# Kernel tuning notes

Measured on AMD Instinct MI355X. Metric: run time of the kernel, lower is better.

## Reference

```python
import jax, jax.numpy as jnp
import numpy as np

N = 100000   # total nodes
E = 1600000  # total edges
B = 256      # graphs per batch
F_NODE, F_EDGE, H = 35, 10, 64
N_CONV = 3
IN_DIM = 2 * H + F_EDGE  # 138
EPS = 1e-5


def setup_inputs() -> dict:
    key = jax.random.key(0)
    ks = jax.random.split(key, 16)
    node_features = jax.random.normal(ks[0], (N, F_NODE), dtype=jnp.float32)
    edge_index = jax.random.randint(ks[1], (2, E), 0, N, dtype=jnp.int64)
    edge_features = jax.random.uniform(ks[2], (E, F_EDGE), dtype=jnp.float32)
    graph_index = jnp.sort(jax.random.randint(ks[3], (N,), 0, B, dtype=jnp.int64))
    s = lambda fan_in: 1.0 / np.sqrt(fan_in)
    embed_w = jax.random.uniform(ks[4], (F_NODE, H), jnp.float32, -s(F_NODE), s(F_NODE))
    embed_b = jax.random.uniform(ks[5], (H,), jnp.float32, -s(F_NODE), s(F_NODE))
    gate_w = jax.random.uniform(ks[6], (N_CONV, IN_DIM, H), jnp.float32, -s(IN_DIM), s(IN_DIM))
    gate_b = jax.random.uniform(ks[7], (N_CONV, H), jnp.float32, -s(IN_DIM), s(IN_DIM))
    cand_w = jax.random.uniform(ks[8], (N_CONV, IN_DIM, H), jnp.float32, -s(IN_DIM), s(IN_DIM))
    cand_b = jax.random.uniform(ks[9], (N_CONV, H), jnp.float32, -s(IN_DIM), s(IN_DIM))
    bn_g = jnp.ones((N_CONV, H), dtype=jnp.float32)
    bn_b = jnp.zeros((N_CONV, H), dtype=jnp.float32)
    mlp_w1 = jax.random.uniform(ks[10], (H, 128), jnp.float32, -s(H), s(H))
    mlp_b1 = jax.random.uniform(ks[11], (128,), jnp.float32, -s(H), s(H))
    mlp_w2 = jax.random.uniform(ks[12], (128, 64), jnp.float32, -s(128), s(128))
    mlp_b2 = jax.random.uniform(ks[13], (64,), jnp.float32, -s(128), s(128))
    mlp_w3 = jax.random.uniform(ks[14], (64, 1), jnp.float32, -s(64), s(64))
    mlp_b3 = jax.random.uniform(ks[15], (1,), jnp.float32, -s(64), s(64))
    return dict(node_features=node_features, edge_index=edge_index,
                edge_features=edge_features, graph_index=graph_index,
                embed_w=embed_w, embed_b=embed_b,
                gate_w=gate_w, gate_b=gate_b, cand_w=cand_w, cand_b=cand_b,
                bn_g=bn_g, bn_b=bn_b,
                mlp_w1=mlp_w1, mlp_b1=mlp_b1, mlp_w2=mlp_w2, mlp_b2=mlp_b2,
                mlp_w3=mlp_w3, mlp_b3=mlp_b3)


def _conv(h, src, dst, edge_feat, gw, gb, cw, cb, gamma, beta):
    # gather -> concat -> gated message
    z = jnp.concatenate([h[src], h[dst], edge_feat], axis=1)  # [E, 2H+F_edge]
    g = jax.nn.sigmoid(z @ gw + gb)
    c = jax.nn.softplus(z @ cw + cb)
    m = g * c
    # scatter-add onto source nodes
    agg = jax.ops.segment_sum(m, src, num_segments=h.shape[0])
    # BatchNorm1d (training-mode batch stats, biased variance)
    mu = agg.mean(axis=0)
    var = agg.var(axis=0)
    agg_bn = (agg - mu) * jax.lax.rsqrt(var + EPS) * gamma + beta
    return jax.nn.softplus(h + agg_bn)


def reference(node_features, edge_index, edge_features, graph_index,
              embed_w, embed_b, gate_w, gate_b, cand_w, cand_b, bn_g, bn_b,
              mlp_w1, mlp_b1, mlp_w2, mlp_b2, mlp_w3, mlp_b3):
    src, dst = edge_index[0], edge_index[1]
    h = node_features @ embed_w + embed_b  # [N, H]
    for i in range(N_CONV):
        h = _conv(h, src, dst, edge_features,
                  gate_w[i], gate_b[i], cand_w[i], cand_b[i], bn_g[i], bn_b[i])
    # mean pool per graph (B is static = 256)
    pooled = jax.ops.segment_sum(h, graph_index, num_segments=B)
    counts = jax.ops.segment_sum(jnp.ones((h.shape[0],), h.dtype), graph_index, num_segments=B)
    pooled = pooled / jnp.clip(counts, 1.0, None)[:, None]
    x = jax.nn.softplus(pooled @ mlp_w1 + mlp_b1)
    x = jax.nn.softplus(x @ mlp_w2 + mlp_b2)
    return (x @ mlp_w3 + mlp_b3)[:, 0]  # [B]
```

## Files before the change

### kernel.cpp

```cpp
#include <hip/hip_runtime.h>
#include <hip/hip_bf16.h>

#define NN 100000
#define EE 1600000
#define BB 256
#define F_NODE 35
#define F_EDGE 10
#define HH 64
#define IN_DIM 138
#define N_CONV 3
#define EPSBN 1e-5f
#define NB1 ((NN + 255) / 256)

#define NBLK 6144
#define NGROUPS 17
#define SUBLEN 68
#define EPB 272
#define EPADTOT (NBLK * EPB)
#define NPAD (EPADTOT - EE)
#define EFSTR 12

#define LOG2E 1.442695041f
#define LN2   0.6931471806f

typedef _Float16 half8 __attribute__((ext_vector_type(8)));
typedef float floatx4 __attribute__((ext_vector_type(4)));

__device__ __forceinline__ float softplus_fast(float x) {
    float t = __builtin_amdgcn_exp2f(fminf(LOG2E * x, 126.0f));
    return LN2 * __builtin_amdgcn_logf(1.0f + t);
}
__device__ __forceinline__ float mpair_pre(float g2, float c2) {
    float tg = __builtin_amdgcn_exp2f(g2);
    float sig = __builtin_amdgcn_rcpf(1.0f + tg);
    float tc = __builtin_amdgcn_exp2f(fminf(c2, 126.0f));
    float l = __builtin_amdgcn_logf(1.0f + tc);
    return sig * l;
}

__global__ __launch_bounds__(256)
void hist_rank_kernel(const int* __restrict__ src, int* __restrict__ cnt,
                      int* __restrict__ rank) {
    int e = blockIdx.x * 256 + threadIdx.x;
    rank[e] = atomicAdd(&cnt[src[e]], 1);
}

__global__ __launch_bounds__(256)
void scan1_kernel(int* __restrict__ cnt, int* __restrict__ bsum, int n) {
    __shared__ int ls[256];
    int t = threadIdx.x;
    int i = blockIdx.x * 256 + t;
    int v = (i < n) ? cnt[i] : 0;
    ls[t] = v;
    __syncthreads();
#pragma unroll
    for (int off = 1; off < 256; off <<= 1) {
        int add = (t >= off) ? ls[t - off] : 0;
        __syncthreads();
        ls[t] += add;
        __syncthreads();
    }
    if (i < n) cnt[i] = ls[t] - v;
    if (t == 255) bsum[blockIdx.x] = ls[255];
}

__global__ __launch_bounds__(512)
void scan2_kernel(int* __restrict__ bsum, int nb) {
    __shared__ int ls[512];
    int t = threadIdx.x;
    int v = (t < nb) ? bsum[t] : 0;
    ls[t] = v;
    __syncthreads();
#pragma unroll
    for (int off = 1; off < 512; off <<= 1) {
        int add = (t >= off) ? ls[t - off] : 0;
        __syncthreads();
        ls[t] += add;
        __syncthreads();
    }
    if (t < nb) bsum[t] = ls[t] - v;
}

__global__ __launch_bounds__(256)
void perm_kernel(const int* __restrict__ src, const int* __restrict__ rank,
                 const int* __restrict__ offs, const int* __restrict__ bsum,
                 int* __restrict__ perm) {
    int e = blockIdx.x * 256 + threadIdx.x;
    int s = src[e];
    perm[offs[s] + bsum[s >> 8] + rank[e]] = e;
}

__global__ __launch_bounds__(256)
void gather_kernel(const int* __restrict__ perm,
                   const int* __restrict__ src, const int* __restrict__ dst,
                   const float* __restrict__ ef,
                   int* __restrict__ ssorted, int2* __restrict__ sdsorted,
                   _Float16* __restrict__ ef16) {
    int pos = blockIdx.x * 256 + threadIdx.x;
    int e = perm[pos];
    int s = src[e], d = dst[e];
    ssorted[pos] = s;
    int2 sd; sd.x = s; sd.y = d;
    sdsorted[pos] = sd;
    const float2* efe = (const float2*)(ef + (size_t)e * F_EDGE);
    uint* op = (uint*)(ef16 + (size_t)pos * EFSTR);
#pragma unroll
    for (int i = 0; i < 5; i++) {
        float2 v = efe[i];
        _Float16 h0 = (_Float16)v.x;
        _Float16 h1 = (_Float16)v.y;
        op[i] = (uint)*(unsigned short*)&h0 | ((uint)*(unsigned short*)&h1 << 16);
    }
    op[5] = 0u;
}

__global__ __launch_bounds__(256)
void pad_kernel(int* __restrict__ ssorted, int2* __restrict__ sdsorted,
                _Float16* __restrict__ ef16, _Float16* __restrict__ h16) {
    int t = blockIdx.x * 256 + threadIdx.x;
    int pos = EE + t;
    ssorted[pos] = NN;
    int2 sd; sd.x = NN; sd.y = NN;
    sdsorted[pos] = sd;
    uint2 z2; z2.x = 0u; z2.y = 0u;
    uint2* op = (uint2*)(ef16 + (size_t)pos * EFSTR);
    op[0] = z2; op[1] = z2; op[2] = z2;
    if (t < 32) ((uint2*)(h16 + (size_t)NN * HH))[t] = z2;
}

__global__ __launch_bounds__(256)
void prep_w_kernel(const float* __restrict__ gw, const float* __restrict__ cw,
                   _Float16* __restrict__ wT) {
    int idx = blockIdx.x * 256 + threadIdx.x;
    if (idx >= 3 * 128 * 160) return;
    int k = idx % 160;
    int n = (idx / 160) & 127;
    int layer = idx / (160 * 128);
    float v = 0.f;
    if (k < IN_DIM)
        v = (n < 64) ? (-LOG2E) * gw[layer * IN_DIM * HH + k * HH + n]
                     : ( LOG2E) * cw[layer * IN_DIM * HH + k * HH + (n - 64)];
    wT[idx] = (_Float16)v;
}

__global__ __launch_bounds__(256)
void embed_kernel(const float* __restrict__ nf, const float* __restrict__ w,
                  const float* __restrict__ bias, _Float16* __restrict__ h16, int n) {
    __shared__ float wl[F_NODE * HH];
    int tid = threadIdx.x;
    for (int i = tid; i < F_NODE * HH; i += 256) wl[i] = w[i];
    __syncthreads();
    int idx = blockIdx.x * 256 + tid;
    int node = idx >> 6, j = idx & 63;
    if (node >= n) return;
    float acc = bias[j];
    const float* row = nf + node * F_NODE;
#pragma unroll
    for (int k = 0; k < F_NODE; k++) acc += row[k] * wl[k * HH + j];
    h16[idx] = (_Float16)acc;
}

__device__ __forceinline__ void loadA(uint4* A,
                                      const _Float16* __restrict__ h16,
                                      const _Float16* __restrict__ ef16,
                                      int s, int d, int eg, int quad) {
    const uint4* hs = (const uint4*)(h16 + (size_t)s * HH);
    const uint4* hd = (const uint4*)(h16 + (size_t)d * HH);
    A[0] = hs[quad];
    A[1] = hs[quad + 4];
    A[2] = hd[quad];
    A[3] = hd[quad + 4];
    uint4 z; z.x = z.y = z.z = z.w = 0u;
    A[4] = z;
    const _Float16* p = ef16 + (size_t)eg * EFSTR;
    if (quad == 0) {
        uint2 a = *(const uint2*)p;
        uint2 b = *(const uint2*)(p + 4);
        A[4].x = a.x; A[4].y = a.y; A[4].z = b.x; A[4].w = b.y;
    } else if (quad == 1) {
        uint2 a = *(const uint2*)(p + 8);
        A[4].x = a.x; A[4].y = a.y;
    }
}

__global__ __launch_bounds__(128, 3)
void edge_conv_mfma(const _Float16* __restrict__ h16,
                    const int* __restrict__ ssorted,
                    const int2* __restrict__ sdsorted,
                    const _Float16* __restrict__ ef16,
                    const _Float16* __restrict__ wT,
                    const float* __restrict__ gb, const float* __restrict__ cb,
                    float* __restrict__ agg) {
    int lane = threadIdx.x & 63;
    int w = threadIdx.x >> 6;
    int quad = lane >> 4, n15 = lane & 15;
    int blockE = blockIdx.x * EPB;
    int base = blockE + ((n15 >> 2) * SUBLEN) + (n15 & 3);
    int ebase_epi = blockE + quad * SUBLEN;

    int tg = 2 * w;
    half8 B[4][5];
#pragma unroll
    for (int j = 0; j < 2; j++) {
        const _Float16* wrg = wT + ((tg + j) * 16 + n15) * 160 + quad * 8;
        const _Float16* wrc = wT + ((4 + tg + j) * 16 + n15) * 160 + quad * 8;
#pragma unroll
        for (int ks = 0; ks < 5; ks++) {
            B[j][ks]     = *(const half8*)(wrg + ks * 32);
            B[2 + j][ks] = *(const half8*)(wrc + ks * 32);
        }
    }
    float gb0 = -LOG2E * gb[tg * 16 + n15], gb1 = -LOG2E * gb[(tg + 1) * 16 + n15];
    float cb0 =  LOG2E * cb[tg * 16 + n15], cb1 =  LOG2E * cb[(tg + 1) * 16 + n15];
    int colbase = tg * 16 + n15;

    int sprev = -1;
    float am0 = 0.f, am1 = 0.f;

    uint4 A[5];
    {
        int2 sd0 = sdsorted[base];
        loadA(A, h16, ef16, sd0.x, sd0.y, base, quad);
    }
    int2 sdn = sdsorted[base + 4];

    for (int g = 0; g < NGROUPS; g++) {
        int4 ss = *(const int4*)&ssorted[ebase_epi + g * 4];

        floatx4 acc[4];
        acc[0] = (floatx4){gb0, gb0, gb0, gb0};
        acc[1] = (floatx4){gb1, gb1, gb1, gb1};
        acc[2] = (floatx4){cb0, cb0, cb0, cb0};
        acc[3] = (floatx4){cb1, cb1, cb1, cb1};

#pragma unroll
        for (int ks = 0; ks < 5; ks++) {
            half8 a = __builtin_bit_cast(half8, A[ks]);
#pragma unroll
            for (int t = 0; t < 4; t++)
                acc[t] = __builtin_amdgcn_mfma_f32_16x16x32_f16(a, B[t][ks], acc[t], 0, 0, 0);
        }

        int gl = (g + 1 < NGROUPS) ? g + 1 : NGROUPS - 1;
        loadA(A, h16, ef16, sdn.x, sdn.y, base + gl * 4, quad);
        int gp = (g + 2 < NGROUPS) ? g + 2 : NGROUPS - 1;
        sdn = sdsorted[base + gp * 4];

        float mm0[4], mm1[4];
#pragma unroll
        for (int r = 0; r < 4; r++) {
            mm0[r] = mpair_pre(acc[0][r], acc[2][r]);
            mm1[r] = mpair_pre(acc[1][r], acc[3][r]);
        }
        int srr[4] = {ss.x, ss.y, ss.z, ss.w};
#pragma unroll
        for (int r = 0; r < 4; r++) {
            int sr = srr[r];
            if (sr != sprev) {
                if (sprev >= 0) {
                    float* p = agg + (size_t)sprev * HH + colbase;
                    atomicAdd(p, am0);
                    atomicAdd(p + 16, am1);
                }
                sprev = sr;
                am0 = am1 = 0.f;
            }
            am0 = fmaf(mm0[r], LN2, am0);
            am1 = fmaf(mm1[r], LN2, am1);
        }
    }
    if (sprev >= 0) {
        float* p = agg + (size_t)sprev * HH + colbase;
        atomicAdd(p, am0);
        atomicAdd(p + 16, am1);
    }
}

__global__ __launch_bounds__(256)
void bn_stats_kernel(const float* __restrict__ agg, float* __restrict__ stats, int total) {
    __shared__ float ls[256], lss[256];
    int tid = threadIdx.x;
    float s = 0.f, ss = 0.f;
    for (int idx = blockIdx.x * 256 + tid; idx < total; idx += gridDim.x * 256) {
        float v = agg[idx];
        s += v;
        ss += v * v;
    }
    ls[tid] = s;
    lss[tid] = ss;
    __syncthreads();
    if (tid < 64) {
        s = ls[tid] + ls[tid + 64] + ls[tid + 128] + ls[tid + 192];
        ss = lss[tid] + lss[tid + 64] + lss[tid + 128] + lss[tid + 192];
        atomicAdd(&stats[tid], s);
        atomicAdd(&stats[64 + tid], ss);
    }
}

__global__ __launch_bounds__(256)
void bn_update_kernel(_Float16* __restrict__ h16,
                      float* __restrict__ agg,
                      const float* __restrict__ stats,
                      const float* __restrict__ g, const float* __restrict__ b,
                      int total, float invN) {
    int idx = blockIdx.x * 256 + threadIdx.x;
    if (idx >= total) return;
    int j = idx & 63;
    float mu = stats[j] * invN;
    float var = stats[64 + j] * invN - mu * mu;
    var = fmaxf(var, 0.0f);
    float scale = g[j] * rsqrtf(var + EPSBN);
    float a = agg[idx];
    agg[idx] = 0.f;
    float v = (float)h16[idx] + (a - mu) * scale + b[j];
    h16[idx] = (_Float16)softplus_fast(v);
}

__global__ __launch_bounds__(256)
void pool_kernel(const _Float16* __restrict__ h16, const int* __restrict__ gi,
                 float* __restrict__ pool, float* __restrict__ counts, int n) {
    int tid = threadIdx.x;
    int grp = tid >> 6;
    int j = tid & 63;
    int n0 = blockIdx.x * 64 + grp * 16;
    if (n0 >= n) return;
    int nend = n0 + 16; if (nend > n) nend = n;
    int gprev = gi[n0];
    float a = 0.f;
    int cnt = 0;
    for (int nn = n0; nn < nend; nn++) {
        int gg = gi[nn];
        if (gg != gprev) {
            atomicAdd(&pool[gprev * 64 + j], a);
            if (j == 0) atomicAdd(&counts[gprev], (float)cnt);
            a = 0.f; cnt = 0; gprev = gg;
        }
        a += (float)h16[(size_t)nn * 64 + j];
        cnt++;
    }
    atomicAdd(&pool[gprev * 64 + j], a);
    if (j == 0) atomicAdd(&counts[gprev], (float)cnt);
}

__global__ __launch_bounds__(128)
void mlp_kernel(const float* __restrict__ pool, const float* __restrict__ counts,
                const float* __restrict__ w1, const float* __restrict__ b1,
                const float* __restrict__ w2, const float* __restrict__ b2,
                const float* __restrict__ w3, const float* __restrict__ b3,
                float* __restrict__ out) {
    __shared__ float x0[64], x1[128], x2[64];
    int b = blockIdx.x, t = threadIdx.x;
    if (t < 64) {
        float c = counts[b];
        c = c < 1.f ? 1.f : c;
        x0[t] = pool[b * 64 + t] / c;
    }
    __syncthreads();
    {
        float acc = 0.f;
#pragma unroll
        for (int k = 0; k < 64; k++) acc += x0[k] * w1[k * 128 + t];
        x1[t] = softplus_fast(acc + b1[t]);
    }
    __syncthreads();
    if (t < 64) {
        float acc = 0.f;
#pragma unroll
        for (int k = 0; k < 128; k++) acc += x1[k] * w2[k * 64 + t];
        x2[t] = softplus_fast(acc + b2[t]);
    }
    __syncthreads();
    if (t == 0) {
        float acc = 0.f;
        for (int k = 0; k < 64; k++) acc += x2[k] * w3[k];
        out[b] = acc + b3[0];
    }
}

extern "C" void kernel_launch(void* const* d_in, const int* in_sizes, int n_in,
                              void* d_out, int out_size, void* d_ws, size_t ws_size,
                              hipStream_t stream) {
    const float* nf      = (const float*)d_in[0];
    const int*   ei      = (const int*)d_in[1];
    const float* ef      = (const float*)d_in[2];
    const int*   gi      = (const int*)d_in[3];
    const float* embed_w = (const float*)d_in[4];
    const float* embed_b = (const float*)d_in[5];
    const float* gate_w  = (const float*)d_in[6];
    const float* gate_b  = (const float*)d_in[7];
    const float* cand_w  = (const float*)d_in[8];
    const float* cand_b  = (const float*)d_in[9];
    const float* bn_g    = (const float*)d_in[10];
    const float* bn_b    = (const float*)d_in[11];
    const float* w1      = (const float*)d_in[12];
    const float* b1      = (const float*)d_in[13];
    const float* w2      = (const float*)d_in[14];
    const float* b2      = (const float*)d_in[15];
    const float* w3      = (const float*)d_in[16];
    const float* b3      = (const float*)d_in[17];
    float* out = (float*)d_out;

    const int NH = NN * HH;
    char* p = (char*)d_ws;
    int*       offs    = (int*)p;              p += (size_t)NN * 4;
    float*     agg     = (float*)p;            p += (size_t)(NN + 1) * HH * 4;
    float*     stats   = (float*)p;            p += 3 * 128 * 4;
    float*     pool    = (float*)p;            p += (size_t)BB * HH * 4;
    float*     counts  = (float*)p;            p += (size_t)BB * 4;
    size_t zero_bytes = (size_t)(p - (char*)d_ws);
    _Float16*  h16     = (_Float16*)p;         p += (size_t)(NN + 1) * HH * 2;
    int*       ssorted = (int*)p;              p += (size_t)EPADTOT * 4;
    int2*      sdsorted= (int2*)p;             p += (size_t)EPADTOT * 8;
    _Float16*  ef16    = (_Float16*)p;         p += (size_t)EPADTOT * EFSTR * 2;
    int*       perm    = (int*)p;              p += (size_t)EE * 4;
    int*       rank    = (int*)p;              p += (size_t)EE * 4;
    _Float16*  wTall   = (_Float16*)p;         p += (size_t)3 * 128 * 160 * 2;
    int*       bsum    = (int*)p;              p += 512 * 4;

    const int* src = ei;
    const int* dst = ei + EE;

    hipMemsetAsync(d_ws, 0, zero_bytes, stream);

    hist_rank_kernel<<<EE / 256, 256, 0, stream>>>(src, offs, rank);
    prep_w_kernel<<<(3 * 128 * 160 + 255) / 256, 256, 0, stream>>>(gate_w, cand_w, wTall);
    pad_kernel<<<NPAD / 256, 256, 0, stream>>>(ssorted, sdsorted, ef16, h16);
    scan1_kernel<<<NB1, 256, 0, stream>>>(offs, bsum, NN);
    scan2_kernel<<<1, 512, 0, stream>>>(bsum, NB1);
    perm_kernel<<<EE / 256, 256, 0, stream>>>(src, rank, offs, bsum, perm);
    gather_kernel<<<EE / 256, 256, 0, stream>>>(perm, src, dst, ef, ssorted, sdsorted, ef16);

    embed_kernel<<<NH / 256, 256, 0, stream>>>(nf, embed_w, embed_b, h16, NN);

    for (int i = 0; i < N_CONV; i++) {
        edge_conv_mfma<<<NBLK, 128, 0, stream>>>(
            h16, ssorted, sdsorted, ef16,
            wTall + (size_t)i * 128 * 160,
            gate_b + i * HH, cand_b + i * HH, agg);
        bn_stats_kernel<<<512, 256, 0, stream>>>(agg, stats + i * 128, NH);
        bn_update_kernel<<<NH / 256, 256, 0, stream>>>(
            h16, agg, stats + i * 128, bn_g + i * HH, bn_b + i * HH, NH, 1.0f / (float)NN);
    }

    pool_kernel<<<(NN + 63) / 64, 256, 0, stream>>>(h16, gi, pool, counts, NN);
    mlp_kernel<<<BB, 128, 0, stream>>>(pool, counts, w1, b1, w2, b2, w3, b3, out);
}
```

Measured before the change: 964.8 us.

## Double-buffer edge gathers two groups ahead and enlarge per-block edge tiles

Halves the block count and doubles edges per block (34 groups of 4 per sub-lane), so the per-block weight-fragment loads and the final atomic flush are amortised over more edges. The main loop is unrolled by two with two A buffers, prefetching gathered node/edge rows two groups ahead and indices four ahead to hide gather latency. The occupancy hint in launch bounds is removed and the padding sentinel check becomes an unsigned range test. Extra registers for the second buffer may lower occupancy, and fewer blocks may balance less evenly across CUs.

```diff
diff --git a/kernel.cpp b/kernel.cpp
--- a/kernel.cpp
+++ b/kernel.cpp
@@ -12,10 +12,10 @@
 #define EPSBN 1e-5f
 #define NB1 ((NN + 255) / 256)
 
-#define NBLK 6144
-#define NGROUPS 17
-#define SUBLEN 68
-#define EPB 272
+#define NBLK 3072
+#define NGROUPS 34
+#define SUBLEN 136
+#define EPB 544
 #define EPADTOT (NBLK * EPB)
 #define NPAD (EPADTOT - EE)
 #define EFSTR 12
@@ -183,7 +183,7 @@
     }
 }
 
-__global__ __launch_bounds__(128, 3)
+__global__ __launch_bounds__(128)
 void edge_conv_mfma(const _Float16* __restrict__ h16,
                     const int* __restrict__ ssorted,
                     const int2* __restrict__ sdsorted,
@@ -217,59 +217,69 @@
     int sprev = -1;
     float am0 = 0.f, am1 = 0.f;
 
-    uint4 A[5];
+    uint4 A0[5], A1[5];
+    int2 sdn0, sdn1;
     {
-        int2 sd0 = sdsorted[base];
-        loadA(A, h16, ef16, sd0.x, sd0.y, base, quad);
-    }
-    int2 sdn = sdsorted[base + 4];
-
-    for (int g = 0; g < NGROUPS; g++) {
-        int4 ss = *(const int4*)&ssorted[ebase_epi + g * 4];
-
-        floatx4 acc[4];
-        acc[0] = (floatx4){gb0, gb0, gb0, gb0};
-        acc[1] = (floatx4){gb1, gb1, gb1, gb1};
-        acc[2] = (floatx4){cb0, cb0, cb0, cb0};
-        acc[3] = (floatx4){cb1, cb1, cb1, cb1};
-
-#pragma unroll
-        for (int ks = 0; ks < 5; ks++) {
-            half8 a = __builtin_bit_cast(half8, A[ks]);
-#pragma unroll
-            for (int t = 0; t < 4; t++)
-                acc[t] = __builtin_amdgcn_mfma_f32_16x16x32_f16(a, B[t][ks], acc[t], 0, 0, 0);
+        int2 a = sdsorted[base];
+        int2 b = sdsorted[base + 4];
+        loadA(A0, h16, ef16, a.x, a.y, base, quad);
+        loadA(A1, h16, ef16, b.x, b.y, base + 4, quad);
+        sdn0 = sdsorted[base + 8];
+        sdn1 = sdsorted[base + 12];
+    }
+
+    for (int g = 0; g < NGROUPS; g += 2) {
+#pragma unroll
+        for (int k = 0; k < 2; k++) {
+            int gk = g + k;
+            int4 ss = *(const int4*)&ssorted[ebase_epi + gk * 4];
+
+            floatx4 acc[4];
+            acc[0] = (floatx4){gb0, gb0, gb0, gb0};
+            acc[1] = (floatx4){gb1, gb1, gb1, gb1};
+            acc[2] = (floatx4){cb0, cb0, cb0, cb0};
+            acc[3] = (floatx4){cb1, cb1, cb1, cb1};
+
+#pragma unroll
+            for (int ks = 0; ks < 5; ks++) {
+                half8 a = __builtin_bit_cast(half8, k == 0 ? A0[ks] : A1[ks]);
+#pragma unroll
+                for (int t = 0; t < 4; t++)
+                    acc[t] = __builtin_amdgcn_mfma_f32_16x16x32_f16(a, B[t][ks], acc[t], 0, 0, 0);
+            }
+
+            int gl = (gk + 2 < NGROUPS) ? gk + 2 : NGROUPS - 1;
+            if (k == 0) loadA(A0, h16, ef16, sdn0.x, sdn0.y, base + gl * 4, quad);
+            else        loadA(A1, h16, ef16, sdn1.x, sdn1.y, base + gl * 4, quad);
+            int gp = (gk + 4 < NGROUPS) ? gk + 4 : NGROUPS - 1;
+            int2 sdf = sdsorted[base + gp * 4];
+            if (k == 0) sdn0 = sdf; else sdn1 = sdf;
+
+            float mm0[4], mm1[4];
+#pragma unroll
+            for (int r = 0; r < 4; r++) {
+                mm0[r] = mpair_pre(acc[0][r], acc[2][r]);
+                mm1[r] = mpair_pre(acc[1][r], acc[3][r]);
+            }
+            int srr[4] = {ss.x, ss.y, ss.z, ss.w};
+#pragma unroll
+            for (int r = 0; r < 4; r++) {
+                int sr = srr[r];
+                if (sr != sprev) {
+                    if ((unsigned)sprev < (unsigned)NN) {
+                        float* p = agg + (size_t)sprev * HH + colbase;
+                        atomicAdd(p, am0);
+                        atomicAdd(p + 16, am1);
+                    }
+                    sprev = sr;
+                    am0 = am1 = 0.f;
+                }
+                am0 = fmaf(mm0[r], LN2, am0);
+                am1 = fmaf(mm1[r], LN2, am1);
+            }
         }
-
-        int gl = (g + 1 < NGROUPS) ? g + 1 : NGROUPS - 1;
-        loadA(A, h16, ef16, sdn.x, sdn.y, base + gl * 4, quad);
-        int gp = (g + 2 < NGROUPS) ? g + 2 : NGROUPS - 1;
-        sdn = sdsorted[base + gp * 4];
-
-        float mm0[4], mm1[4];
-#pragma unroll
-        for (int r = 0; r < 4; r++) {
-            mm0[r] = mpair_pre(acc[0][r], acc[2][r]);
-            mm1[r] = mpair_pre(acc[1][r], acc[3][r]);
-        }
-        int srr[4] = {ss.x, ss.y, ss.z, ss.w};
-#pragma unroll
-        for (int r = 0; r < 4; r++) {
-            int sr = srr[r];
-            if (sr != sprev) {
-                if (sprev >= 0) {
-                    float* p = agg + (size_t)sprev * HH + colbase;
-                    atomicAdd(p, am0);
-                    atomicAdd(p + 16, am1);
-                }
-                sprev = sr;
-                am0 = am1 = 0.f;
-            }
-            am0 = fmaf(mm0[r], LN2, am0);
-            am1 = fmaf(mm1[r], LN2, am1);
-        }
-    }
-    if (sprev >= 0) {
+    }
+    if ((unsigned)sprev < (unsigned)NN) {
         float* p = agg + (size_t)sprev * HH + colbase;
         atomicAdd(p, am0);
         atomicAdd(p + 16, am1);
```

After: 852.0 us. 1.13x faster.

## Fuse prep, scan, BN and pool+MLP kernels using grid barriers; double edge block size

Applied to the files above, without the earlier changes.

Merges the embed, histogram, weight-prep and pad kernels into one multi-role launch, and the two scans into one using a last-block-done pattern. BN stats and update are fused with a spin-based grid barrier over 512 blocks, and pooling and the MLP are fused the same way. It also halves the edge-conv block count while doubling edges per block, and filters padding sources with an unsigned bound check. The aim is fewer launches and launch gaps. The cost is spin-barrier risk, since every block must be co-resident, and a different per-block load balance in the edge conv.

```diff
diff --git a/kernel.cpp b/kernel.cpp
--- a/kernel.cpp
+++ b/kernel.cpp
@@ -12,13 +12,21 @@
 #define EPSBN 1e-5f
 #define NB1 ((NN + 255) / 256)
 
-#define NBLK 6144
-#define NGROUPS 17
-#define SUBLEN 68
-#define EPB 272
+#define NBLK 3072
+#define NGROUPS 34
+#define SUBLEN 136
+#define EPB 544
 #define EPADTOT (NBLK * EPB)
 #define NPAD (EPADTOT - EE)
 #define EFSTR 12
+
+#define PREP_EMBED_BLKS 25000
+#define PREP_HIST_BLKS  6250
+#define PREP_W_BLKS     240
+#define PREP_PAD_BLKS   278
+#define PREP_TOT (PREP_EMBED_BLKS + PREP_HIST_BLKS + PREP_W_BLKS + PREP_PAD_BLKS)
+
+#define SYNC_GRID 512
 
 #define LOG2E 1.442695041f
 #define LN2   0.6931471806f
@@ -38,19 +46,71 @@
     return sig * l;
 }
 
-__global__ __launch_bounds__(256)
-void hist_rank_kernel(const int* __restrict__ src, int* __restrict__ cnt,
-                      int* __restrict__ rank) {
-    int e = blockIdx.x * 256 + threadIdx.x;
-    rank[e] = atomicAdd(&cnt[src[e]], 1);
-}
-
-__global__ __launch_bounds__(256)
-void scan1_kernel(int* __restrict__ cnt, int* __restrict__ bsum, int n) {
+__device__ __forceinline__ void grid_barrier(int* counter, int nblocks) {
+    __syncthreads();
+    if (threadIdx.x == 0) {
+        __hip_atomic_fetch_add(counter, 1, __ATOMIC_ACQ_REL, __HIP_MEMORY_SCOPE_AGENT);
+        while (__hip_atomic_load(counter, __ATOMIC_ACQUIRE, __HIP_MEMORY_SCOPE_AGENT) < nblocks)
+            __builtin_amdgcn_s_sleep(8);
+    }
+    __syncthreads();
+}
+
+__global__ __launch_bounds__(256)
+void prep_kernel(const float* __restrict__ nf, const float* __restrict__ ew,
+                 const float* __restrict__ eb, _Float16* __restrict__ h16,
+                 const int* __restrict__ src, int* __restrict__ cnt, int* __restrict__ rank,
+                 const float* __restrict__ gw, const float* __restrict__ cw,
+                 _Float16* __restrict__ wT,
+                 int* __restrict__ ssorted, int2* __restrict__ sdsorted,
+                 _Float16* __restrict__ ef16) {
+    int bid = blockIdx.x;
+    int tid = threadIdx.x;
+    if (bid < PREP_EMBED_BLKS) {
+        __shared__ float wl[F_NODE * HH];
+        for (int i = tid; i < F_NODE * HH; i += 256) wl[i] = ew[i];
+        __syncthreads();
+        int idx = bid * 256 + tid;
+        int node = idx >> 6, j = idx & 63;
+        if (node >= NN) return;
+        float acc = eb[j];
+        const float* row = nf + node * F_NODE;
+#pragma unroll
+        for (int k = 0; k < F_NODE; k++) acc += row[k] * wl[k * HH + j];
+        h16[idx] = (_Float16)acc;
+    } else if (bid < PREP_EMBED_BLKS + PREP_HIST_BLKS) {
+        int e = (bid - PREP_EMBED_BLKS) * 256 + tid;
+        rank[e] = atomicAdd(&cnt[src[e]], 1);
+    } else if (bid < PREP_EMBED_BLKS + PREP_HIST_BLKS + PREP_W_BLKS) {
+        int idx = (bid - PREP_EMBED_BLKS - PREP_HIST_BLKS) * 256 + tid;
+        int k = idx % 160;
+        int n = (idx / 160) & 127;
+        int layer = idx / (160 * 128);
+        float v = 0.f;
+        if (k < IN_DIM)
+            v = (n < 64) ? (-LOG2E) * gw[layer * IN_DIM * HH + k * HH + n]
+                         : ( LOG2E) * cw[layer * IN_DIM * HH + k * HH + (n - 64)];
+        wT[idx] = (_Float16)v;
+    } else {
+        int t = (bid - PREP_EMBED_BLKS - PREP_HIST_BLKS - PREP_W_BLKS) * 256 + tid;
+        int pos = EE + t;
+        ssorted[pos] = NN;
+        int2 sd; sd.x = NN; sd.y = NN;
+        sdsorted[pos] = sd;
+        uint2 z2; z2.x = 0u; z2.y = 0u;
+        uint2* op = (uint2*)(ef16 + (size_t)pos * EFSTR);
+        op[0] = z2; op[1] = z2; op[2] = z2;
+        if (t < 32) ((uint2*)(h16 + (size_t)NN * HH))[t] = z2;
+    }
+}
+
+__global__ __launch_bounds__(256)
+void scan_kernel(int* __restrict__ cnt, int* __restrict__ bsum, int* __restrict__ done) {
     __shared__ int ls[256];
+    __shared__ int lastflag;
     int t = threadIdx.x;
     int i = blockIdx.x * 256 + t;
-    int v = (i < n) ? cnt[i] : 0;
+    int v = (i < NN) ? cnt[i] : 0;
     ls[t] = v;
     __syncthreads();
 #pragma unroll
@@ -60,25 +120,31 @@
         ls[t] += add;
         __syncthreads();
     }
-    if (i < n) cnt[i] = ls[t] - v;
-    if (t == 255) bsum[blockIdx.x] = ls[255];
-}
-
-__global__ __launch_bounds__(512)
-void scan2_kernel(int* __restrict__ bsum, int nb) {
-    __shared__ int ls[512];
-    int t = threadIdx.x;
-    int v = (t < nb) ? bsum[t] : 0;
-    ls[t] = v;
+    if (i < NN) cnt[i] = ls[t] - v;
+    if (t == 255)
+        __hip_atomic_store(&bsum[blockIdx.x], ls[255], __ATOMIC_RELEASE, __HIP_MEMORY_SCOPE_AGENT);
+    __syncthreads();
+    if (t == 0) {
+        int old = __hip_atomic_fetch_add(done, 1, __ATOMIC_ACQ_REL, __HIP_MEMORY_SCOPE_AGENT);
+        lastflag = (old == NB1 - 1);
+    }
+    __syncthreads();
+    if (!lastflag) return;
+    __shared__ int bs[512];
+    int v0 = (t < NB1) ? __hip_atomic_load(&bsum[t], __ATOMIC_ACQUIRE, __HIP_MEMORY_SCOPE_AGENT) : 0;
+    int v1 = (256 + t < NB1) ? __hip_atomic_load(&bsum[256 + t], __ATOMIC_ACQUIRE, __HIP_MEMORY_SCOPE_AGENT) : 0;
+    bs[t] = v0; bs[256 + t] = v1;
     __syncthreads();
 #pragma unroll
     for (int off = 1; off < 512; off <<= 1) {
-        int add = (t >= off) ? ls[t - off] : 0;
+        int a0 = bs[t];       int add0 = (t >= off) ? bs[t - off] : 0;
+        int a1 = bs[256 + t]; int add1 = (256 + t >= off) ? bs[256 + t - off] : 0;
         __syncthreads();
-        ls[t] += add;
+        bs[t] = a0 + add0; bs[256 + t] = a1 + add1;
         __syncthreads();
     }
-    if (t < nb) bsum[t] = ls[t] - v;
+    if (t < NB1) bsum[t] = (t == 0) ? 0 : bs[t - 1];
+    if (256 + t < NB1) bsum[256 + t] = bs[256 + t - 1];
 }
 
 __global__ __launch_bounds__(256)
@@ -112,52 +178,6 @@
         op[i] = (uint)*(unsigned short*)&h0 | ((uint)*(unsigned short*)&h1 << 16);
     }
     op[5] = 0u;
-}
-
-__global__ __launch_bounds__(256)
-void pad_kernel(int* __restrict__ ssorted, int2* __restrict__ sdsorted,
-                _Float16* __restrict__ ef16, _Float16* __restrict__ h16) {
-    int t = blockIdx.x * 256 + threadIdx.x;
-    int pos = EE + t;
-    ssorted[pos] = NN;
-    int2 sd; sd.x = NN; sd.y = NN;
-    sdsorted[pos] = sd;
-    uint2 z2; z2.x = 0u; z2.y = 0u;
-    uint2* op = (uint2*)(ef16 + (size_t)pos * EFSTR);
-    op[0] = z2; op[1] = z2; op[2] = z2;
-    if (t < 32) ((uint2*)(h16 + (size_t)NN * HH))[t] = z2;
-}
-
-__global__ __launch_bounds__(256)
-void prep_w_kernel(const float* __restrict__ gw, const float* __restrict__ cw,
-                   _Float16* __restrict__ wT) {
-    int idx = blockIdx.x * 256 + threadIdx.x;
-    if (idx >= 3 * 128 * 160) return;
-    int k = idx % 160;
-    int n = (idx / 160) & 127;
-    int layer = idx / (160 * 128);
-    float v = 0.f;
-    if (k < IN_DIM)
-        v = (n < 64) ? (-LOG2E) * gw[layer * IN_DIM * HH + k * HH + n]
-                     : ( LOG2E) * cw[layer * IN_DIM * HH + k * HH + (n - 64)];
-    wT[idx] = (_Float16)v;
-}
-
-__global__ __launch_bounds__(256)
-void embed_kernel(const float* __restrict__ nf, const float* __restrict__ w,
-                  const float* __restrict__ bias, _Float16* __restrict__ h16, int n) {
-    __shared__ float wl[F_NODE * HH];
-    int tid = threadIdx.x;
-    for (int i = tid; i < F_NODE * HH; i += 256) wl[i] = w[i];
-    __syncthreads();
-    int idx = blockIdx.x * 256 + tid;
-    int node = idx >> 6, j = idx & 63;
-    if (node >= n) return;
-    float acc = bias[j];
-    const float* row = nf + node * F_NODE;
-#pragma unroll
-    for (int k = 0; k < F_NODE; k++) acc += row[k] * wl[k * HH + j];
-    h16[idx] = (_Float16)acc;
 }
 
 __device__ __forceinline__ void loadA(uint4* A,
@@ -257,7 +277,7 @@
         for (int r = 0; r < 4; r++) {
             int sr = srr[r];
             if (sr != sprev) {
-                if (sprev >= 0) {
+                if ((unsigned)sprev < (unsigned)NN) {
                     float* p = agg + (size_t)sprev * HH + colbase;
                     atomicAdd(p, am0);
                     atomicAdd(p + 16, am1);
@@ -269,7 +289,7 @@
             am1 = fmaf(mm1[r], LN2, am1);
         }
     }
-    if (sprev >= 0) {
+    if ((unsigned)sprev < (unsigned)NN) {
         float* p = agg + (size_t)sprev * HH + colbase;
         atomicAdd(p, am0);
         atomicAdd(p + 16, am1);
@@ -277,11 +297,14 @@
 }
 
 __global__ __launch_bounds__(256)
-void bn_stats_kernel(const float* __restrict__ agg, float* __restrict__ stats, int total) {
+void bn_fused_kernel(_Float16* __restrict__ h16, float* __restrict__ agg,
+                     float* __restrict__ stats,
+                     const float* __restrict__ g, const float* __restrict__ b,
+                     int* __restrict__ counter, float invN) {
     __shared__ float ls[256], lss[256];
     int tid = threadIdx.x;
     float s = 0.f, ss = 0.f;
-    for (int idx = blockIdx.x * 256 + tid; idx < total; idx += gridDim.x * 256) {
+    for (int idx = blockIdx.x * 256 + tid; idx < NN * HH; idx += SYNC_GRID * 256) {
         float v = agg[idx];
         s += v;
         ss += v * v;
@@ -295,82 +318,79 @@
         atomicAdd(&stats[tid], s);
         atomicAdd(&stats[64 + tid], ss);
     }
-}
-
-__global__ __launch_bounds__(256)
-void bn_update_kernel(_Float16* __restrict__ h16,
-                      float* __restrict__ agg,
-                      const float* __restrict__ stats,
-                      const float* __restrict__ g, const float* __restrict__ b,
-                      int total, float invN) {
-    int idx = blockIdx.x * 256 + threadIdx.x;
-    if (idx >= total) return;
-    int j = idx & 63;
-    float mu = stats[j] * invN;
-    float var = stats[64 + j] * invN - mu * mu;
-    var = fmaxf(var, 0.0f);
+    grid_barrier(counter, SYNC_GRID);
+    int j = tid & 63;
+    float sj  = __hip_atomic_load(&stats[j], __ATOMIC_RELAXED, __HIP_MEMORY_SCOPE_AGENT);
+    float ssj = __hip_atomic_load(&stats[64 + j], __ATOMIC_RELAXED, __HIP_MEMORY_SCOPE_AGENT);
+    float mu = sj * invN;
+    float var = fmaxf(ssj * invN - mu * mu, 0.0f);
     float scale = g[j] * rsqrtf(var + EPSBN);
-    float a = agg[idx];
-    agg[idx] = 0.f;
-    float v = (float)h16[idx] + (a - mu) * scale + b[j];
-    h16[idx] = (_Float16)softplus_fast(v);
-}
-
-__global__ __launch_bounds__(256)
-void pool_kernel(const _Float16* __restrict__ h16, const int* __restrict__ gi,
-                 float* __restrict__ pool, float* __restrict__ counts, int n) {
+    float bj = b[j];
+    for (int idx = blockIdx.x * 256 + tid; idx < NN * HH; idx += SYNC_GRID * 256) {
+        float a = agg[idx];
+        agg[idx] = 0.f;
+        float v = (float)h16[idx] + (a - mu) * scale + bj;
+        h16[idx] = (_Float16)softplus_fast(v);
+    }
+}
+
+__global__ __launch_bounds__(256)
+void poolmlp_kernel(const _Float16* __restrict__ h16, const int* __restrict__ gi,
+                    float* __restrict__ pool, float* __restrict__ counts,
+                    int* __restrict__ counter,
+                    const float* __restrict__ w1, const float* __restrict__ b1,
+                    const float* __restrict__ w2, const float* __restrict__ b2,
+                    const float* __restrict__ w3, const float* __restrict__ b3,
+                    float* __restrict__ out) {
     int tid = threadIdx.x;
     int grp = tid >> 6;
     int j = tid & 63;
-    int n0 = blockIdx.x * 64 + grp * 16;
-    if (n0 >= n) return;
-    int nend = n0 + 16; if (nend > n) nend = n;
-    int gprev = gi[n0];
-    float a = 0.f;
-    int cnt = 0;
-    for (int nn = n0; nn < nend; nn++) {
-        int gg = gi[nn];
-        if (gg != gprev) {
-            atomicAdd(&pool[gprev * 64 + j], a);
-            if (j == 0) atomicAdd(&counts[gprev], (float)cnt);
-            a = 0.f; cnt = 0; gprev = gg;
+    for (int sb = blockIdx.x; sb < (NN + 63) / 64; sb += SYNC_GRID) {
+        int n0 = sb * 64 + grp * 16;
+        if (n0 >= NN) continue;
+        int nend = n0 + 16; if (nend > NN) nend = NN;
+        int gprev = gi[n0];
+        float a = 0.f;
+        int cnt = 0;
+        for (int nn = n0; nn < nend; nn++) {
+            int gg = gi[nn];
+            if (gg != gprev) {
+                atomicAdd(&pool[gprev * 64 + j], a);
+                if (j == 0) atomicAdd(&counts[gprev], (float)cnt);
+                a = 0.f; cnt = 0; gprev = gg;
+            }
+            a += (float)h16[(size_t)nn * 64 + j];
+            cnt++;
         }
-        a += (float)h16[(size_t)nn * 64 + j];
-        cnt++;
-    }
-    atomicAdd(&pool[gprev * 64 + j], a);
-    if (j == 0) atomicAdd(&counts[gprev], (float)cnt);
-}
-
-__global__ __launch_bounds__(128)
-void mlp_kernel(const float* __restrict__ pool, const float* __restrict__ counts,
-                const float* __restrict__ w1, const float* __restrict__ b1,
-                const float* __restrict__ w2, const float* __restrict__ b2,
-                const float* __restrict__ w3, const float* __restrict__ b3,
-                float* __restrict__ out) {
+        atomicAdd(&pool[gprev * 64 + j], a);
+        if (j == 0) atomicAdd(&counts[gprev], (float)cnt);
+    }
+    grid_barrier(counter, SYNC_GRID);
+    if (blockIdx.x >= BB) return;
+    int b = blockIdx.x;
     __shared__ float x0[64], x1[128], x2[64];
-    int b = blockIdx.x, t = threadIdx.x;
-    if (t < 64) {
-        float c = counts[b];
+    if (tid < 64) {
+        float c = __hip_atomic_load(&counts[b], __ATOMIC_RELAXED, __HIP_MEMORY_SCOPE_AGENT);
         c = c < 1.f ? 1.f : c;
-        x0[t] = pool[b * 64 + t] / c;
-    }
-    __syncthreads();
-    {
+        float pv = __hip_atomic_load(&pool[b * 64 + tid], __ATOMIC_RELAXED, __HIP_MEMORY_SCOPE_AGENT);
+        x0[tid] = pv / c;
+    }
+    __syncthreads();
+    if (tid < 128) {
         float acc = 0.f;
 #pragma unroll
-        for (int k = 0; k < 64; k++) acc += x0[k] * w1[k * 128 + t];
-        x1[t] = softplus_fast(acc + b1[t]);
-    }
-    __syncthreads();
-    if (t < 64) {
+        for (int k = 0; k < 64; k++) acc += x0[k] * w1[k * 128 + tid];
+        x1[tid] = softplus_fast(acc + b1[tid]);
+    }
+    __syncthreads();
+    if (tid < 64) {
         float acc = 0.f;
 #pragma unroll
-        for (int k = 0; k < 128; k++) acc += x1[k] * w2[k * 64 + t];
-        x2[t] = softplus_fast(acc + b2[t]);
-    }
-    __syncthreads();
-    if (t == 0) {
+        for (int k = 0; k < 128; k++) acc += x1[k] * w2[k * 64 + tid];
+        x2[tid] = softplus_fast(acc + b2[tid]);
+    }
+    __syncthreads();
+    if (tid == 0) {
         float acc = 0.f;
         for (int k = 0; k < 64; k++) acc += x2[k] * w3[k];
         out[b] = acc + b3[0];
@@ -407,6 +427,7 @@
     float*     stats   = (float*)p;            p += 3 * 128 * 4;
     float*     pool    = (float*)p;            p += (size_t)BB * HH * 4;
     float*     counts  = (float*)p;            p += (size_t)BB * 4;
+    int*       sync    = (int*)p;              p += 8 * 4;
     size_t zero_bytes = (size_t)(p - (char*)d_ws);
     _Float16*  h16     = (_Float16*)p;         p += (size_t)(NN + 1) * HH * 2;
     int*       ssorted = (int*)p;              p += (size_t)EPADTOT * 4;
@@ -422,26 +443,25 @@
 
     hipMemsetAsync(d_ws, 0, zero_bytes, stream);
 
-    hist_rank_kernel<<<EE / 256, 256, 0, stream>>>(src, offs, rank);
-    prep_w_kernel<<<(3 * 128 * 160 + 255) / 256, 256, 0, stream>>>(gate_w, cand_w, wTall);
-    pad_kernel<<<NPAD / 256, 256, 0, stream>>>(ssorted, sdsorted, ef16, h16);
-    scan1_kernel<<<NB1, 256, 0, stream>>>(offs, bsum, NN);
-    scan2_kernel<<<1, 512, 0, stream>>>(bsum, NB1);
+    prep_kernel<<<PREP_TOT, 256, 0, stream>>>(
+        nf, embed_w, embed_b, h16, src, offs, rank,
+        gate_w, cand_w, wTall, ssorted, sdsorted, ef16);
+
+    scan_kernel<<<NB1, 256, 0, stream>>>(offs, bsum, sync + 4);
+
     perm_kernel<<<EE / 256, 256, 0, stream>>>(src, rank, offs, bsum, perm);
     gather_kernel<<<EE / 256, 256, 0, stream>>>(perm, src, dst, ef, ssorted, sdsorted, ef16);
-
-    embed_kernel<<<NH / 256, 256, 0, stream>>>(nf, embed_w, embed_b, h16, NN);
 
     for (int i = 0; i < N_CONV; i++) {
         edge_conv_mfma<<<NBLK, 128, 0, stream>>>(
             h16, ssorted, sdsorted, ef16,
             wTall + (size_t)i * 128 * 160,
             gate_b + i * HH, cand_b + i * HH, agg);
-        bn_stats_kernel<<<512, 256, 0, stream>>>(agg, stats + i * 128, NH);
-        bn_update_kernel<<<NH / 256, 256, 0, stream>>>(
-            h16, agg, stats + i * 128, bn_g + i * HH, bn_b + i * HH, NH, 1.0f / (float)NN);
-    }
-
-    pool_kernel<<<(NN + 63) / 64, 256, 0, stream>>>(h16, gi, pool, counts, NN);
-    mlp_kernel<<<BB, 128, 0, stream>>>(pool, counts, w1, b1, w2, b2, w3, b3, out);
-}
+        bn_fused_kernel<<<SYNC_GRID, 256, 0, stream>>>(
+            h16, agg, stats + i * 128, bn_g + i * HH, bn_b + i * HH,
+            sync + i, 1.0f / (float)NN);
+    }
+
+    poolmlp_kernel<<<SYNC_GRID, 256, 0, stream>>>(
+        h16, gi, pool, counts, sync + 3, w1, b1, w2, b2, w3, b3, out);
+}
```

Result: slower. 1.013 ms (+5.0%).
